# Performance work log

Measured on AMD Instinct MI355X. Metric: run time of the kernel, lower is better.

Reference implementation:

```python
import jax, jax.numpy as jnp
import numpy as np

# Dimensions: N sites, B batch, D bond dim, d physical dim, C output classes
N, B, D, d, C = 1024, 256, 16, 2, 10
STDDEV = 1e-5
INIT_DIAG = 1.0


def setup_inputs() -> dict:
    key = jax.random.key(0)
    k1, k2, k3 = jax.random.split(key, 3)
    x = jax.random.normal(k1, (N, B, d), dtype=jnp.float32)
    eye = jnp.eye(D, dtype=jnp.float32)
    # tensor[n,:,:,i] = init_diag * I + stddev * noise  (matches TF init)
    tensor = INIT_DIAG * eye[None, :, :, None] + STDDEV * jax.random.normal(k2, (N, D, D, d), dtype=jnp.float32)
    # Aout[c] = I + stddev * noise
    Aout = eye[None, :, :] + STDDEV * jax.random.normal(k3, (C, D, D), dtype=jnp.float32)
    return {"x": x, "tensor": tensor, "Aout": Aout}


def _chain_prod(A):
    # A: (n, b, D, D) -> ordered matrix-chain product (b, D, D), log-depth tree.
    # Faithful to parallel_contract: pairwise einsum per level; odd leftover is
    # kept at the end of the list (order-preserving, associativity-equivalent).
    while A.shape[0] > 1:
        n = A.shape[0]
        half = n // 2
        prod = jnp.einsum('nblk,nbkr->nblr', A[0:2 * half:2], A[1:2 * half:2])
        if n % 2 == 1:
            prod = jnp.concatenate([prod, A[-1:]], axis=0)
        A = prod
    return A[0]


def reference(x, tensor, Aout):
    # A: (N, B, D, D) site matrices after contracting input features
    A = jnp.einsum('nbi,nlri->nblr', x, tensor)
    nhalf = A.shape[0] // 2
    # Left half product, take row 0 (left boundary); right half, take col 0
    Al = _chain_prod(A[:nhalf])[:, 0, :]   # (B, D)
    Ar = _chain_prod(A[nhalf:])[:, :, 0]   # (B, D)
    # out[b,o] = Al[b] @ Aout[o] @ Ar[b]
    return jnp.einsum('bl,olr,br->bo', Al, Aout, Ar)
```

## Files before the change

### kernel.cpp

```cpp
#include <hip/hip_runtime.h>


#define BATCH  256
#define NCLS   10
#define NSITES 1024
#define NGRP   16
#define SEGLEN 16
#define NB     8

typedef __attribute__((ext_vector_type(4))) float f32x4;
typedef __attribute__((ext_vector_type(4))) short short4b;
typedef __attribute__((ext_vector_type(2))) unsigned uint2v;
typedef __attribute__((ext_vector_type(4))) unsigned uint4v;
typedef __attribute__((ext_vector_type(4))) unsigned short us4;

static __device__ __forceinline__ unsigned short bf16tr(float f) {
    return (unsigned short)(__builtin_bit_cast(unsigned, f) >> 16);
}
static __device__ __forceinline__ unsigned short bf16rne(float f) {
    unsigned u = __builtin_bit_cast(unsigned, f);
    u += 0x7FFFu + ((u >> 16) & 1u);
    return (unsigned short)(u >> 16);
}
static __device__ __forceinline__ float bf16tof(unsigned short h) {
    return __builtin_bit_cast(float, (unsigned)h << 16);
}
static __device__ __forceinline__ unsigned fbits(float f) {
    return __builtin_bit_cast(unsigned, f);
}
static __device__ __forceinline__ float lo16(unsigned u) {
    return __builtin_bit_cast(float, u << 16);
}
static __device__ __forceinline__ float hi16(unsigned u) {
    return __builtin_bit_cast(float, u & 0xffff0000u);
}
static __device__ __forceinline__ unsigned pkhi(float hi, float lo) {
    return __builtin_amdgcn_perm(fbits(hi), fbits(lo), 0x07060302u);
}
static __device__ __forceinline__ short4b mk4(unsigned lo, unsigned hi) {
    uint2v u; u.x = lo; u.y = hi;
    return __builtin_bit_cast(short4b, u);
}
static __device__ __forceinline__ f32x4 mfma16(short4b a, short4b b, f32x4 c) {
#if __has_builtin(__builtin_amdgcn_mfma_f32_16x16x16bf16_1k)
    return __builtin_amdgcn_mfma_f32_16x16x16bf16_1k(a, b, c, 0, 0, 0);
#else
    f32x4 d;
    asm volatile("v_mfma_f32_16x16x16_bf16 %0, %1, %2, %3"
                 : "=v"(d) : "v"(a), "v"(b), "v"(c));
    return d;
#endif
}

__global__ __launch_bounds__(256) void ta_pack_kernel(
    const float* __restrict__ tensor, unsigned short* __restrict__ Ta)
{
    __shared__ float s[512];
    const int n = blockIdx.x, t = threadIdx.x;
    *(float2*)(s + 2 * t) = *(const float2*)(tensor + (size_t)n * 512 + 2 * t);
    __syncthreads();
    const int o0 = 2 * t;
    const int lane = o0 >> 3, e0 = o0 & 7;
    const int q = lane >> 4, m = lane & 15;
    const int i = e0 >> 2, j0 = e0 & 3;
    const int k0 = 4 * q + j0;
    const float v0 = s[k0 * 32 + m * 2 + i];
    const float v1 = s[(k0 + 1) * 32 + m * 2 + i];
    ((unsigned*)Ta)[(size_t)n * 256 + t] =
        (unsigned)bf16rne(v0) | ((unsigned)bf16rne(v1) << 16);
}

__global__ __launch_bounds__(256) void chain_kernel(
    const float* __restrict__ x,
    const unsigned short* __restrict__ Ta,
    unsigned short* __restrict__ M2)
{
    __shared__ __align__(16) unsigned short rm[32 * 256];
    __shared__ __align__(16) unsigned short cm[32 * 256];
    const int t = threadIdx.x, wave = t >> 6, lane = t & 63;
    const int quad = lane >> 4, l15 = lane & 15;
    const int bt = blockIdx.x & 31, g = blockIdx.x >> 5;
    const int b0 = bt * NB;
    const int seg = g * 4 + wave, n0 = seg * SEGLEN;

    f32x4 d[NB];
#pragma unroll
    for (int j = 0; j < NB; ++j)
#pragma unroll
        for (int r = 0; r < 4; ++r) d[j][r] = (quad * 4 + r == l15) ? 1.0f : 0.0f;

    const uint4v* __restrict__ tp = (const uint4v*)Ta + (size_t)n0 * 64 + lane;

#pragma unroll 4
    for (int s = 0; s < SEGLEN; ++s) {
        const int n = n0 + s;
        const uint4v tw = tp[(size_t)s * 64];
        const float2* __restrict__ xv = (const float2*)(x + ((size_t)n * BATCH + b0) * 2);
        float2 xs[NB];
#pragma unroll
        for (int j = 0; j < NB; ++j) xs[j] = xv[j];
        const float t00 = lo16(tw.x), t01 = hi16(tw.x), t02 = lo16(tw.y), t03 = hi16(tw.y);
        const float t10 = lo16(tw.z), t11 = hi16(tw.z), t12 = lo16(tw.w), t13 = hi16(tw.w);
#pragma unroll
        for (int j = 0; j < NB; ++j) {
            const float a0 = __builtin_fmaf(xs[j].x, t00, xs[j].y * t10);
            const float a1 = __builtin_fmaf(xs[j].x, t01, xs[j].y * t11);
            const float a2 = __builtin_fmaf(xs[j].x, t02, xs[j].y * t12);
            const float a3 = __builtin_fmaf(xs[j].x, t03, xs[j].y * t13);
            const short4b af = mk4(pkhi(a1, a0), pkhi(a3, a2));
            const short4b bf = mk4(pkhi(d[j][1], d[j][0]), pkhi(d[j][3], d[j][2]));
            f32x4 c0 = {0.0f, 0.0f, 0.0f, 0.0f};
            d[j] = mfma16(af, bf, c0);
        }
    }

    if (wave & 1) {
#pragma unroll
        for (int j = 0; j < NB; ++j) {
            const int sl = j * 4 + wave;
#pragma unroll
            for (int r = 0; r < 4; ++r)
                rm[sl * 256 + (quad * 4 + r) * 16 + l15] = bf16tr(d[j][r]);
        }
    } else {
#pragma unroll
        for (int j = 0; j < NB; ++j) {
            const int sl = j * 4 + wave;
            us4 pk = {bf16tr(d[j][0]), bf16tr(d[j][1]), bf16tr(d[j][2]), bf16tr(d[j][3])};
            *(us4*)(cm + sl * 256 + l15 * 16 + quad * 4) = pk;
        }
    }
    __syncthreads();

    short4b af1[4], bf1[4];
#pragma unroll
    for (int i = 0; i < 4; ++i) {
        const int p = 4 * wave + i, j = p >> 1, h = p & 1;
        af1[i] = __builtin_bit_cast(short4b,
            *(const uint2v*)(rm + (j * 4 + 2 * h + 1) * 256 + l15 * 16 + quad * 4));
        bf1[i] = __builtin_bit_cast(short4b,
            *(const uint2v*)(cm + (j * 4 + 2 * h) * 256 + l15 * 16 + quad * 4));
    }
    __syncthreads();
#pragma unroll
    for (int i = 0; i < 4; ++i) {
        const int p = 4 * wave + i, j = p >> 1, h = p & 1;
        f32x4 c0 = {0.0f, 0.0f, 0.0f, 0.0f};
        f32x4 q = mfma16(af1[i], bf1[i], c0);
        const int sl = j * 4 + h;
        if (h) {
#pragma unroll
            for (int r = 0; r < 4; ++r)
                rm[sl * 256 + (quad * 4 + r) * 16 + l15] = bf16tr(q[r]);
        } else {
            us4 pk = {bf16tr(q[0]), bf16tr(q[1]), bf16tr(q[2]), bf16tr(q[3])};
            *(us4*)(cm + sl * 256 + l15 * 16 + quad * 4) = pk;
        }
    }
    __syncthreads();

#pragma unroll
    for (int i = 0; i < 2; ++i) {
        const int j = 2 * wave + i;
        const short4b af2 = __builtin_bit_cast(short4b,
            *(const uint2v*)(rm + (j * 4 + 1) * 256 + l15 * 16 + quad * 4));
        const short4b bf2 = __builtin_bit_cast(short4b,
            *(const uint2v*)(cm + (j * 4 + 0) * 256 + l15 * 16 + quad * 4));
        f32x4 c0 = {0.0f, 0.0f, 0.0f, 0.0f};
        f32x4 rr = mfma16(af2, bf2, c0);
        us4 pk = {bf16tr(rr[0]), bf16tr(rr[1]), bf16tr(rr[2]), bf16tr(rr[3])};
        *(us4*)(M2 + ((size_t)(b0 + j) * NGRP + g) * 256 + l15 * 16 + quad * 4) = pk;
    }
}

__global__ __launch_bounds__(256) void combine_kernel(
    const unsigned short* __restrict__ M2,
    const float* __restrict__ Aout,
    float* __restrict__ out)
{
    __shared__ __align__(16) unsigned short rm[16 * 256];
    __shared__ __align__(16) unsigned short cm[16 * 256];
    const int b = blockIdx.x, t = threadIdx.x;
    const int wave = t >> 6, lane = t & 63, quad = lane >> 4, l15 = lane & 15;
    typedef __attribute__((ext_vector_type(8))) short short8;

    const short8* __restrict__ src = (const short8*)(M2 + (size_t)b * NGRP * 256);
#pragma unroll
    for (int i2 = 0; i2 < 2; ++i2) {
        const int i = t + 256 * i2;
        const short8 v = src[i];
        *((short8*)cm + i) = v;
        const int mat = i >> 5, c = (i >> 1) & 15, r0 = (i & 1) * 8;
#pragma unroll
        for (int e = 0; e < 8; ++e)
            rm[mat * 256 + (r0 + e) * 16 + c] = (unsigned short)v[e];
    }
    __syncthreads();

    for (int lvl = 0; lvl < 3; ++lvl) {
        const int np = 8 >> lvl;
        short4b afr[2], bfr[2];
        int pids[2], nmine = 0;
        for (int p = wave; p < np; p += 4) {
            afr[nmine] = __builtin_bit_cast(short4b,
                 *(const uint2v*)(rm + (2 * p + 1) * 256 + l15 * 16 + quad * 4));
            bfr[nmine] = __builtin_bit_cast(short4b,
                 *(const uint2v*)(cm + (2 * p) * 256 + l15 * 16 + quad * 4));
            pids[nmine] = p; ++nmine;
        }
        __syncthreads();
        for (int ii = 0; ii < nmine; ++ii) {
            f32x4 c0 = {0.0f, 0.0f, 0.0f, 0.0f};
            f32x4 r = mfma16(afr[ii], bfr[ii], c0);
            const int p = pids[ii];
#pragma unroll
            for (int rr = 0; rr < 4; ++rr)
                rm[p * 256 + (quad * 4 + rr) * 16 + l15] = bf16tr(r[rr]);
            us4 pk = {bf16tr(r[0]), bf16tr(r[1]), bf16tr(r[2]), bf16tr(r[3])};
            *(us4*)(cm + p * 256 + l15 * 16 + quad * 4) = pk;
        }
        __syncthreads();
    }

    if (t < NCLS * 16) {
        const int o = t >> 4, r = t & 15;
        const float vr = bf16tof(rm[256 + r]);
        float s = 0.0f;
#pragma unroll
        for (int l = 0; l < 16; ++l)
            s = __builtin_fmaf(bf16tof(rm[l * 16]), Aout[((size_t)o * 16 + l) * 16 + r], s);
        s *= vr;
#pragma unroll
        for (int off = 8; off > 0; off >>= 1)
            s += __shfl_xor(s, off, 16);
        if (r == 0) out[(size_t)b * NCLS + o] = s;
    }
}

extern "C" void kernel_launch(void* const* d_in, const int* in_sizes, int n_in,
                              void* d_out, int out_size, void* d_ws, size_t ws_size,
                              hipStream_t stream)
{
    const float* x      = (const float*)d_in[0];
    const float* tensor = (const float*)d_in[1];
    const float* Aout   = (const float*)d_in[2];
    float* out = (float*)d_out;

    unsigned short* Ta = (unsigned short*)d_ws;
    unsigned short* M2 = (unsigned short*)((char*)d_ws + (1 << 20));

    ta_pack_kernel<<<NSITES, 256, 0, stream>>>(tensor, Ta);
    chain_kernel<<<BATCH * NGRP / NB, 256, 0, stream>>>(x, Ta, M2);
    combine_kernel<<<BATCH, 256, 0, stream>>>(M2, Aout, out);
}
```

Measured before the change: 77.14 us.

## Fuse pack, chain and combine into one cooperative kernel with grid sync

Replaces the three kernel launches with one cooperative launch of 512 blocks. The chain phase now reads fp32 tensor directly and contracts over the physical index after the MFMA: two MFMAs per site, one per tensor slice, are combined with x via FMA. A grid-wide sync separates it from the combine phase. This removes the separate packing pass, its workspace traffic and launch overheads, but doubles MFMA work per site and adds a grid barrier.

```diff
diff --git a/kernel.cpp b/kernel.cpp
--- a/kernel.cpp
+++ b/kernel.cpp
@@ -1,4 +1,5 @@
 #include <hip/hip_runtime.h>
+#include <hip/hip_cooperative_groups.h>
 
 
 #define BATCH  256
@@ -7,32 +8,24 @@
 #define NGRP   16
 #define SEGLEN 16
 #define NB     8
+#define NBLK   512
+
+namespace cg = cooperative_groups;
 
 typedef __attribute__((ext_vector_type(4))) float f32x4;
 typedef __attribute__((ext_vector_type(4))) short short4b;
 typedef __attribute__((ext_vector_type(2))) unsigned uint2v;
-typedef __attribute__((ext_vector_type(4))) unsigned uint4v;
 typedef __attribute__((ext_vector_type(4))) unsigned short us4;
+typedef __attribute__((ext_vector_type(8))) short short8;
 
 static __device__ __forceinline__ unsigned short bf16tr(float f) {
     return (unsigned short)(__builtin_bit_cast(unsigned, f) >> 16);
 }
-static __device__ __forceinline__ unsigned short bf16rne(float f) {
-    unsigned u = __builtin_bit_cast(unsigned, f);
-    u += 0x7FFFu + ((u >> 16) & 1u);
-    return (unsigned short)(u >> 16);
-}
 static __device__ __forceinline__ float bf16tof(unsigned short h) {
     return __builtin_bit_cast(float, (unsigned)h << 16);
 }
 static __device__ __forceinline__ unsigned fbits(float f) {
     return __builtin_bit_cast(unsigned, f);
-}
-static __device__ __forceinline__ float lo16(unsigned u) {
-    return __builtin_bit_cast(float, u << 16);
-}
-static __device__ __forceinline__ float hi16(unsigned u) {
-    return __builtin_bit_cast(float, u & 0xffff0000u);
 }
 static __device__ __forceinline__ unsigned pkhi(float hi, float lo) {
     return __builtin_amdgcn_perm(fbits(hi), fbits(lo), 0x07060302u);
@@ -52,188 +45,173 @@
 #endif
 }
 
-__global__ __launch_bounds__(256) void ta_pack_kernel(
-    const float* __restrict__ tensor, unsigned short* __restrict__ Ta)
-{
-    __shared__ float s[512];
-    const int n = blockIdx.x, t = threadIdx.x;
-    *(float2*)(s + 2 * t) = *(const float2*)(tensor + (size_t)n * 512 + 2 * t);
-    __syncthreads();
-    const int o0 = 2 * t;
-    const int lane = o0 >> 3, e0 = o0 & 7;
-    const int q = lane >> 4, m = lane & 15;
-    const int i = e0 >> 2, j0 = e0 & 3;
-    const int k0 = 4 * q + j0;
-    const float v0 = s[k0 * 32 + m * 2 + i];
-    const float v1 = s[(k0 + 1) * 32 + m * 2 + i];
-    ((unsigned*)Ta)[(size_t)n * 256 + t] =
-        (unsigned)bf16rne(v0) | ((unsigned)bf16rne(v1) << 16);
-}
-
-__global__ __launch_bounds__(256) void chain_kernel(
+__global__ __launch_bounds__(256) void fused_kernel(
     const float* __restrict__ x,
-    const unsigned short* __restrict__ Ta,
+    const float* __restrict__ tensor,
+    const float* __restrict__ Aout,
+    float* __restrict__ out,
     unsigned short* __restrict__ M2)
 {
     __shared__ __align__(16) unsigned short rm[32 * 256];
     __shared__ __align__(16) unsigned short cm[32 * 256];
     const int t = threadIdx.x, wave = t >> 6, lane = t & 63;
     const int quad = lane >> 4, l15 = lane & 15;
-    const int bt = blockIdx.x & 31, g = blockIdx.x >> 5;
+    const int bid = blockIdx.x;
+    const int bt = bid & 31, g = bid >> 5;
     const int b0 = bt * NB;
     const int seg = g * 4 + wave, n0 = seg * SEGLEN;
 
-    f32x4 d[NB];
-#pragma unroll
-    for (int j = 0; j < NB; ++j)
-#pragma unroll
-        for (int r = 0; r < 4; ++r) d[j][r] = (quad * 4 + r == l15) ? 1.0f : 0.0f;
-
-    const uint4v* __restrict__ tp = (const uint4v*)Ta + (size_t)n0 * 64 + lane;
+    {
+        f32x4 d[NB];
+#pragma unroll
+        for (int j = 0; j < NB; ++j)
+#pragma unroll
+            for (int r = 0; r < 4; ++r) d[j][r] = (quad * 4 + r == l15) ? 1.0f : 0.0f;
+
+        const float* __restrict__ tb =
+            tensor + (size_t)n0 * 512 + ((size_t)(4 * quad) * 16 + l15) * 2;
 
 #pragma unroll 4
-    for (int s = 0; s < SEGLEN; ++s) {
-        const int n = n0 + s;
-        const uint4v tw = tp[(size_t)s * 64];
-        const float2* __restrict__ xv = (const float2*)(x + ((size_t)n * BATCH + b0) * 2);
-        float2 xs[NB];
-#pragma unroll
-        for (int j = 0; j < NB; ++j) xs[j] = xv[j];
-        const float t00 = lo16(tw.x), t01 = hi16(tw.x), t02 = lo16(tw.y), t03 = hi16(tw.y);
-        const float t10 = lo16(tw.z), t11 = hi16(tw.z), t12 = lo16(tw.w), t13 = hi16(tw.w);
-#pragma unroll
-        for (int j = 0; j < NB; ++j) {
-            const float a0 = __builtin_fmaf(xs[j].x, t00, xs[j].y * t10);
-            const float a1 = __builtin_fmaf(xs[j].x, t01, xs[j].y * t11);
-            const float a2 = __builtin_fmaf(xs[j].x, t02, xs[j].y * t12);
-            const float a3 = __builtin_fmaf(xs[j].x, t03, xs[j].y * t13);
-            const short4b af = mk4(pkhi(a1, a0), pkhi(a3, a2));
-            const short4b bf = mk4(pkhi(d[j][1], d[j][0]), pkhi(d[j][3], d[j][2]));
+        for (int s = 0; s < SEGLEN; ++s) {
+            const float* __restrict__ ts = tb + (size_t)s * 512;
+            const float2 v0 = *(const float2*)(ts);
+            const float2 v1 = *(const float2*)(ts + 32);
+            const float2 v2 = *(const float2*)(ts + 64);
+            const float2 v3 = *(const float2*)(ts + 96);
+            const short4b af0 = mk4(pkhi(v1.x, v0.x), pkhi(v3.x, v2.x));
+            const short4b af1 = mk4(pkhi(v1.y, v0.y), pkhi(v3.y, v2.y));
+            const float4* __restrict__ xp =
+                (const float4*)(x + ((size_t)(n0 + s) * BATCH + b0) * 2);
+            const float4 xq0 = xp[0], xq1 = xp[1], xq2 = xp[2], xq3 = xp[3];
+            const float xs0[NB] = {xq0.x, xq0.z, xq1.x, xq1.z, xq2.x, xq2.z, xq3.x, xq3.z};
+            const float xs1[NB] = {xq0.y, xq0.w, xq1.y, xq1.w, xq2.y, xq2.w, xq3.y, xq3.w};
+#pragma unroll
+            for (int j = 0; j < NB; ++j) {
+                const short4b wb = mk4(pkhi(d[j][1], d[j][0]), pkhi(d[j][3], d[j][2]));
+                const f32x4 z = {0.0f, 0.0f, 0.0f, 0.0f};
+                const f32x4 d0 = mfma16(af0, wb, z);
+                const f32x4 d1 = mfma16(af1, wb, z);
+#pragma unroll
+                for (int r = 0; r < 4; ++r)
+                    d[j][r] = __builtin_fmaf(xs1[j], d1[r], xs0[j] * d0[r]);
+            }
+        }
+
+        if (wave & 1) {
+#pragma unroll
+            for (int j = 0; j < NB; ++j) {
+                const int sl = j * 4 + wave;
+#pragma unroll
+                for (int r = 0; r < 4; ++r)
+                    rm[sl * 256 + (quad * 4 + r) * 16 + l15] = bf16tr(d[j][r]);
+            }
+        } else {
+#pragma unroll
+            for (int j = 0; j < NB; ++j) {
+                const int sl = j * 4 + wave;
+                us4 pk = {bf16tr(d[j][0]), bf16tr(d[j][1]), bf16tr(d[j][2]), bf16tr(d[j][3])};
+                *(us4*)(cm + sl * 256 + l15 * 16 + quad * 4) = pk;
+            }
+        }
+        __syncthreads();
+
+        short4b af1v[4], bf1v[4];
+#pragma unroll
+        for (int i = 0; i < 4; ++i) {
+            const int p = 4 * wave + i, j = p >> 1, h = p & 1;
+            af1v[i] = __builtin_bit_cast(short4b,
+                *(const uint2v*)(rm + (j * 4 + 2 * h + 1) * 256 + l15 * 16 + quad * 4));
+            bf1v[i] = __builtin_bit_cast(short4b,
+                *(const uint2v*)(cm + (j * 4 + 2 * h) * 256 + l15 * 16 + quad * 4));
+        }
+        __syncthreads();
+#pragma unroll
+        for (int i = 0; i < 4; ++i) {
+            const int p = 4 * wave + i, j = p >> 1, h = p & 1;
             f32x4 c0 = {0.0f, 0.0f, 0.0f, 0.0f};
-            d[j] = mfma16(af, bf, c0);
+            f32x4 q = mfma16(af1v[i], bf1v[i], c0);
+            const int sl = j * 4 + h;
+            if (h) {
+#pragma unroll
+                for (int r = 0; r < 4; ++r)
+                    rm[sl * 256 + (quad * 4 + r) * 16 + l15] = bf16tr(q[r]);
+            } else {
+                us4 pk = {bf16tr(q[0]), bf16tr(q[1]), bf16tr(q[2]), bf16tr(q[3])};
+                *(us4*)(cm + sl * 256 + l15 * 16 + quad * 4) = pk;
+            }
+        }
+        __syncthreads();
+
+#pragma unroll
+        for (int i = 0; i < 2; ++i) {
+            const int j = 2 * wave + i;
+            const short4b af2 = __builtin_bit_cast(short4b,
+                *(const uint2v*)(rm + (j * 4 + 1) * 256 + l15 * 16 + quad * 4));
+            const short4b bf2 = __builtin_bit_cast(short4b,
+                *(const uint2v*)(cm + (j * 4 + 0) * 256 + l15 * 16 + quad * 4));
+            f32x4 c0 = {0.0f, 0.0f, 0.0f, 0.0f};
+            f32x4 rr = mfma16(af2, bf2, c0);
+            us4 pk = {bf16tr(rr[0]), bf16tr(rr[1]), bf16tr(rr[2]), bf16tr(rr[3])};
+            *(us4*)(M2 + ((size_t)(b0 + j) * NGRP + g) * 256 + l15 * 16 + quad * 4) = pk;
         }
     }
 
-    if (wave & 1) {
-#pragma unroll
-        for (int j = 0; j < NB; ++j) {
-            const int sl = j * 4 + wave;
-#pragma unroll
-            for (int r = 0; r < 4; ++r)
-                rm[sl * 256 + (quad * 4 + r) * 16 + l15] = bf16tr(d[j][r]);
-        }
-    } else {
-#pragma unroll
-        for (int j = 0; j < NB; ++j) {
-            const int sl = j * 4 + wave;
-            us4 pk = {bf16tr(d[j][0]), bf16tr(d[j][1]), bf16tr(d[j][2]), bf16tr(d[j][3])};
-            *(us4*)(cm + sl * 256 + l15 * 16 + quad * 4) = pk;
-        }
-    }
-    __syncthreads();
-
-    short4b af1[4], bf1[4];
-#pragma unroll
-    for (int i = 0; i < 4; ++i) {
-        const int p = 4 * wave + i, j = p >> 1, h = p & 1;
-        af1[i] = __builtin_bit_cast(short4b,
-            *(const uint2v*)(rm + (j * 4 + 2 * h + 1) * 256 + l15 * 16 + quad * 4));
-        bf1[i] = __builtin_bit_cast(short4b,
-            *(const uint2v*)(cm + (j * 4 + 2 * h) * 256 + l15 * 16 + quad * 4));
-    }
-    __syncthreads();
-#pragma unroll
-    for (int i = 0; i < 4; ++i) {
-        const int p = 4 * wave + i, j = p >> 1, h = p & 1;
-        f32x4 c0 = {0.0f, 0.0f, 0.0f, 0.0f};
-        f32x4 q = mfma16(af1[i], bf1[i], c0);
-        const int sl = j * 4 + h;
-        if (h) {
-#pragma unroll
-            for (int r = 0; r < 4; ++r)
-                rm[sl * 256 + (quad * 4 + r) * 16 + l15] = bf16tr(q[r]);
-        } else {
-            us4 pk = {bf16tr(q[0]), bf16tr(q[1]), bf16tr(q[2]), bf16tr(q[3])};
-            *(us4*)(cm + sl * 256 + l15 * 16 + quad * 4) = pk;
-        }
-    }
-    __syncthreads();
-
-#pragma unroll
-    for (int i = 0; i < 2; ++i) {
-        const int j = 2 * wave + i;
-        const short4b af2 = __builtin_bit_cast(short4b,
-            *(const uint2v*)(rm + (j * 4 + 1) * 256 + l15 * 16 + quad * 4));
-        const short4b bf2 = __builtin_bit_cast(short4b,
-            *(const uint2v*)(cm + (j * 4 + 0) * 256 + l15 * 16 + quad * 4));
-        f32x4 c0 = {0.0f, 0.0f, 0.0f, 0.0f};
-        f32x4 rr = mfma16(af2, bf2, c0);
-        us4 pk = {bf16tr(rr[0]), bf16tr(rr[1]), bf16tr(rr[2]), bf16tr(rr[3])};
-        *(us4*)(M2 + ((size_t)(b0 + j) * NGRP + g) * 256 + l15 * 16 + quad * 4) = pk;
-    }
-}
-
-__global__ __launch_bounds__(256) void combine_kernel(
-    const unsigned short* __restrict__ M2,
-    const float* __restrict__ Aout,
-    float* __restrict__ out)
-{
-    __shared__ __align__(16) unsigned short rm[16 * 256];
-    __shared__ __align__(16) unsigned short cm[16 * 256];
-    const int b = blockIdx.x, t = threadIdx.x;
-    const int wave = t >> 6, lane = t & 63, quad = lane >> 4, l15 = lane & 15;
-    typedef __attribute__((ext_vector_type(8))) short short8;
-
-    const short8* __restrict__ src = (const short8*)(M2 + (size_t)b * NGRP * 256);
-#pragma unroll
-    for (int i2 = 0; i2 < 2; ++i2) {
-        const int i = t + 256 * i2;
-        const short8 v = src[i];
-        *((short8*)cm + i) = v;
-        const int mat = i >> 5, c = (i >> 1) & 15, r0 = (i & 1) * 8;
-#pragma unroll
-        for (int e = 0; e < 8; ++e)
-            rm[mat * 256 + (r0 + e) * 16 + c] = (unsigned short)v[e];
-    }
-    __syncthreads();
-
-    for (int lvl = 0; lvl < 3; ++lvl) {
-        const int np = 8 >> lvl;
-        short4b afr[2], bfr[2];
-        int pids[2], nmine = 0;
-        for (int p = wave; p < np; p += 4) {
-            afr[nmine] = __builtin_bit_cast(short4b,
-                 *(const uint2v*)(rm + (2 * p + 1) * 256 + l15 * 16 + quad * 4));
-            bfr[nmine] = __builtin_bit_cast(short4b,
-                 *(const uint2v*)(cm + (2 * p) * 256 + l15 * 16 + quad * 4));
-            pids[nmine] = p; ++nmine;
-        }
-        __syncthreads();
-        for (int ii = 0; ii < nmine; ++ii) {
-            f32x4 c0 = {0.0f, 0.0f, 0.0f, 0.0f};
-            f32x4 r = mfma16(afr[ii], bfr[ii], c0);
-            const int p = pids[ii];
-#pragma unroll
-            for (int rr = 0; rr < 4; ++rr)
-                rm[p * 256 + (quad * 4 + rr) * 16 + l15] = bf16tr(r[rr]);
-            us4 pk = {bf16tr(r[0]), bf16tr(r[1]), bf16tr(r[2]), bf16tr(r[3])};
-            *(us4*)(cm + p * 256 + l15 * 16 + quad * 4) = pk;
-        }
-        __syncthreads();
-    }
-
-    if (t < NCLS * 16) {
-        const int o = t >> 4, r = t & 15;
-        const float vr = bf16tof(rm[256 + r]);
-        float s = 0.0f;
-#pragma unroll
-        for (int l = 0; l < 16; ++l)
-            s = __builtin_fmaf(bf16tof(rm[l * 16]), Aout[((size_t)o * 16 + l) * 16 + r], s);
-        s *= vr;
-#pragma unroll
-        for (int off = 8; off > 0; off >>= 1)
-            s += __shfl_xor(s, off, 16);
-        if (r == 0) out[(size_t)b * NCLS + o] = s;
+    cg::this_grid().sync();
+
+    if (bid < BATCH) {
+        const int b = bid;
+
+        const short8* __restrict__ src = (const short8*)(M2 + (size_t)b * NGRP * 256);
+#pragma unroll
+        for (int i2 = 0; i2 < 2; ++i2) {
+            const int i = t + 256 * i2;
+            const short8 v = src[i];
+            *((short8*)cm + i) = v;
+            const int mat = i >> 5, c = (i >> 1) & 15, r0 = (i & 1) * 8;
+#pragma unroll
+            for (int e = 0; e < 8; ++e)
+                rm[mat * 256 + (r0 + e) * 16 + c] = (unsigned short)v[e];
+        }
+        __syncthreads();
+
+        for (int lvl = 0; lvl < 3; ++lvl) {
+            const int np = 8 >> lvl;
+            short4b afr[2], bfr[2];
+            int pids[2], nmine = 0;
+            for (int p = wave; p < np; p += 4) {
+                afr[nmine] = __builtin_bit_cast(short4b,
+                     *(const uint2v*)(rm + (2 * p + 1) * 256 + l15 * 16 + quad * 4));
+                bfr[nmine] = __builtin_bit_cast(short4b,
+                     *(const uint2v*)(cm + (2 * p) * 256 + l15 * 16 + quad * 4));
+                pids[nmine] = p; ++nmine;
+            }
+            __syncthreads();
+            for (int ii = 0; ii < nmine; ++ii) {
+                f32x4 c0 = {0.0f, 0.0f, 0.0f, 0.0f};
+                f32x4 r = mfma16(afr[ii], bfr[ii], c0);
+                const int p = pids[ii];
+#pragma unroll
+                for (int rr = 0; rr < 4; ++rr)
+                    rm[p * 256 + (quad * 4 + rr) * 16 + l15] = bf16tr(r[rr]);
+                us4 pk = {bf16tr(r[0]), bf16tr(r[1]), bf16tr(r[2]), bf16tr(r[3])};
+                *(us4*)(cm + p * 256 + l15 * 16 + quad * 4) = pk;
+            }
+            __syncthreads();
+        }
+
+        if (t < NCLS * 16) {
+            const int o = t >> 4, r = t & 15;
+            const float vr = bf16tof(rm[256 + r]);
+            float s = 0.0f;
+#pragma unroll
+            for (int l = 0; l < 16; ++l)
+                s = __builtin_fmaf(bf16tof(rm[l * 16]), Aout[((size_t)o * 16 + l) * 16 + r], s);
+            s *= vr;
+#pragma unroll
+            for (int off = 8; off > 0; off >>= 1)
+                s += __shfl_xor(s, off, 16);
+            if (r == 0) out[(size_t)b * NCLS + o] = s;
+        }
     }
 }
 
@@ -246,10 +224,9 @@
     const float* Aout   = (const float*)d_in[2];
     float* out = (float*)d_out;
 
-    unsigned short* Ta = (unsigned short*)d_ws;
-    unsigned short* M2 = (unsigned short*)((char*)d_ws + (1 << 20));
-
-    ta_pack_kernel<<<NSITES, 256, 0, stream>>>(tensor, Ta);
-    chain_kernel<<<BATCH * NGRP / NB, 256, 0, stream>>>(x, Ta, M2);
-    combine_kernel<<<BATCH, 256, 0, stream>>>(M2, Aout, out);
-}
+    unsigned short* M2 = (unsigned short*)d_ws;
+
+    void* args[] = {(void*)&x, (void*)&tensor, (void*)&Aout, (void*)&out, (void*)&M2};
+    hipLaunchCooperativeKernel((const void*)fused_kernel, dim3(NBLK), dim3(256),
+                               args, 0, stream);
+}
```

New measurement: 132.8 us. 72.2% more time.
